# Kernel tuning notes

Hardware: AMD Instinct MI355X
Metric: run time of the kernel (lower is better)

## Reference

```python
import jax, jax.numpy as jnp
import numpy as np

L, H, P = 32768, 512, 256


def setup_inputs() -> dict:
    key = jax.random.key(0)
    ks = jax.random.split(key, 9)
    sH = 1.0 / np.sqrt(H).astype(np.float32)
    sP = 1.0 / np.sqrt(P).astype(np.float32)
    return {
        "input_sequence": jax.random.normal(ks[0], (L, H), jnp.float32),
        "Lambda_re": jax.random.normal(ks[1], (P,), jnp.float32),
        "Lambda_im": jax.random.normal(ks[2], (P,), jnp.float32) * np.float32(np.pi),
        "B_re": jax.random.normal(ks[3], (P, H), jnp.float32) * sH,
        "B_im": jax.random.normal(ks[4], (P, H), jnp.float32) * sH,
        "C_re": jax.random.normal(ks[5], (H, P), jnp.float32) * sP,
        "C_im": jax.random.normal(ks[6], (H, P), jnp.float32) * sP,
        "D": jax.random.normal(ks[7], (H,), jnp.float32),
        "log_step": jax.random.normal(ks[8], (P,), jnp.float32) - 3.0,
    }


def reference(input_sequence, Lambda_re, Lambda_im, B_re, B_im, C_re, C_im, D, log_step):
    # clip_eigs=True: enforce left-half-plane eigenvalues
    Lambda = jnp.clip(Lambda_re, None, -1e-4) + 1j * Lambda_im          # (P,)
    B_tilde = B_re + 1j * B_im                                          # (P,H)
    C_tilde = C_re + 1j * C_im                                          # (H,P)
    step = jnp.exp(log_step)                                            # step_rescale = 1.0, (P,)

    # ZOH discretization
    Lambda_bar = jnp.exp(Lambda * step)                                 # (P,) complex64
    B_bar = ((Lambda_bar - 1.0) / Lambda)[:, None] * B_tilde            # (P,H) complex64

    # Bu_elements: (L,P) complex; equivalent to vmap(lambda u: B_bar @ u)
    Bu = input_sequence.astype(B_bar.dtype) @ B_bar.T                   # (L,P)
    Lambda_elems = jnp.broadcast_to(Lambda_bar, (input_sequence.shape[0], Lambda_bar.shape[0]))

    def binop(q_i, q_j):
        A_i, b_i = q_i
        A_j, b_j = q_j
        return A_j * A_i, A_j * b_i + b_j

    _, xs = jax.lax.associative_scan(binop, (Lambda_elems, Bu))         # xs: (L,P)

    # conj_sym=True: ys = 2 * Re(C_tilde @ x) per step
    ys = 2.0 * (xs @ C_tilde.T).real                                    # (L,H)
    return ys + D * input_sequence
```

## Files before the change

kernel.cpp:

```cpp
#include <hip/hip_runtime.h>
#include <cstdint>
#include <cstddef>

typedef __bf16 bf16x8 __attribute__((ext_vector_type(8)));
typedef float f32x4 __attribute__((ext_vector_type(4)));

#define L_SEQ 32768
#define H_DIM 512
#define P_DIM 256
#define NP2   512
#define CHUNK 32
#define NCHUNK 1024
#define NSUPER 32

__device__ __forceinline__ void gload_lds16(const void* g, void* l) {
    __builtin_amdgcn_global_load_lds(
        (const __attribute__((address_space(1))) void*)g,
        (__attribute__((address_space(3))) void*)l,
        16, 0, 0);
}

__global__ void prep_kernel(const float* __restrict__ Lre, const float* __restrict__ Lim,
                            const float* __restrict__ lstep, float* __restrict__ par) {
    int p = threadIdx.x;
    if (p >= P_DIM) return;
    float lr = fminf(Lre[p], -1e-4f);
    float li = Lim[p];
    float st = expf(lstep[p]);
    float ldr = lr * st;
    float ldi = li * st;
    float er = expf(ldr);
    float ar = er * cosf(ldi);
    float ai = er * sinf(ldi);
    float den = lr * lr + li * li;
    float mr = ar - 1.0f, mi = ai;
    float cr = (mr * lr + mi * li) / den;
    float ci = (mi * lr - mr * li) / den;
    float e32  = expf((float)CHUNK * ldr);
    float ph32 = (float)CHUNK * ldi;
    float pr = e32 * cosf(ph32);
    float pi = e32 * sinf(ph32);
    par[p] = ar;        par[256 + p] = ai;
    par[512 + p] = cr;  par[768 + p] = ci;
    par[1024 + p] = pr; par[1280 + p] = pi;
    par[1536 + p] = ldr; par[1792 + p] = ldi;
}

__global__ void build_B_kernel(const float* __restrict__ Bre, const float* __restrict__ Bim,
                               const float* __restrict__ par, __bf16* __restrict__ Bt) {
    int idx = blockIdx.x * blockDim.x + threadIdx.x;
    int p = idx >> 9;
    int h = idx & 511;
    float cr = par[512 + p], ci = par[768 + p];
    float br = Bre[idx], bi = Bim[idx];
    Bt[(size_t)p * NP2 + h]         = (__bf16)(cr * br - ci * bi);
    Bt[(size_t)(256 + p) * NP2 + h] = (__bf16)(cr * bi + ci * br);
}

__global__ void build_C_kernel(const float* __restrict__ Cre, const float* __restrict__ Cim,
                               __bf16* __restrict__ Ct) {
    int idx = blockIdx.x * blockDim.x + threadIdx.x;
    int h = idx >> 8;
    int q = idx & 255;
    Ct[(size_t)h * NP2 + q]       = (__bf16)( 2.0f * Cre[idx]);
    Ct[(size_t)h * NP2 + 256 + q] = (__bf16)(-2.0f * Cim[idx]);
}

__global__ void cast_u_kernel(const float4* __restrict__ in, bf16x8* __restrict__ out, int n8) {
    int i = blockIdx.x * blockDim.x + threadIdx.x;
    if (i >= n8) return;
    float4 a = in[2 * i], b = in[2 * i + 1];
    bf16x8 v;
    v[0] = (__bf16)a.x; v[1] = (__bf16)a.y; v[2] = (__bf16)a.z; v[3] = (__bf16)a.w;
    v[4] = (__bf16)b.x; v[5] = (__bf16)b.y; v[6] = (__bf16)b.z; v[7] = (__bf16)b.w;
    out[i] = v;
}

template<bool FUSE>
__global__ __launch_bounds__(256)
void gemm_bt_kernel(const __bf16* __restrict__ A, const __bf16* __restrict__ Bt,
                    void* __restrict__ CoutV, const float* __restrict__ Dvec,
                    const float* __restrict__ U) {
    const int K = NP2, N = NP2;
    __shared__ __align__(16) __bf16 As[2][128 * 64];
    __shared__ __align__(16) __bf16 Bs[2][128 * 64];
    const int t = threadIdx.x;
    const int l = t & 63;
    const int w = t >> 6;
    const int wr = w >> 1, wc = w & 1;
    const int b    = blockIdx.x;
    const int n_sw = (b & 7) * 128 + (b >> 3);
    const int row0 = (n_sw >> 2) * 128;
    const int col0 = (n_sw & 3) * 128;
    const int lr = l & 15;
    const int lk = (l >> 4) * 8;
    f32x4 acc[4][4] = {};

    auto STAGE = [&](int buf, int k0) {
#pragma unroll
        for (int i = 0; i < 4; ++i) {
            int off = i * 256 + t;
            int r  = off >> 3;
            int ce = ((off & 7) ^ (r & 7)) * 8;
            gload_lds16(A  + (size_t)(row0 + r) * K + (k0 + ce), &As[buf][off * 8]);
            gload_lds16(Bt + (size_t)(col0 + r) * K + (k0 + ce), &Bs[buf][off * 8]);
        }
    };

    auto COMPUTE = [&](int buf) {
#pragma unroll
        for (int kk = 0; kk < 64; kk += 32) {
            bf16x8 a[4], b2[4];
            const int ls = (kk + lk) >> 3;
#pragma unroll
            for (int m = 0; m < 4; ++m) {
                int row = wr * 64 + m * 16 + lr;
                a[m] = *reinterpret_cast<const bf16x8*>(&As[buf][row * 64 + ((ls ^ (row & 7)) << 3)]);
            }
#pragma unroll
            for (int n = 0; n < 4; ++n) {
                int row = wc * 64 + n * 16 + lr;
                b2[n] = *reinterpret_cast<const bf16x8*>(&Bs[buf][row * 64 + ((ls ^ (row & 7)) << 3)]);
            }
            __builtin_amdgcn_s_setprio(1);
#pragma unroll
            for (int m = 0; m < 4; ++m)
#pragma unroll
                for (int n = 0; n < 4; ++n)
                    acc[m][n] = __builtin_amdgcn_mfma_f32_16x16x32_bf16(a[m], b2[n], acc[m][n], 0, 0, 0);
            __builtin_amdgcn_s_setprio(0);
        }
    };

    STAGE(0, 0);
    int cur = 0;
#pragma unroll
    for (int k0 = 64; k0 < K; k0 += 64) {
        STAGE(cur ^ 1, k0);
        asm volatile("s_waitcnt vmcnt(8)" ::: "memory");
        __builtin_amdgcn_s_barrier();
        __builtin_amdgcn_sched_barrier(0);
        COMPUTE(cur);
        __builtin_amdgcn_sched_barrier(0);
        __builtin_amdgcn_s_barrier();
        __builtin_amdgcn_sched_barrier(0);
        cur ^= 1;
    }
    asm volatile("s_waitcnt vmcnt(0)" ::: "memory");
    __builtin_amdgcn_s_barrier();
    __builtin_amdgcn_sched_barrier(0);
    COMPUTE(cur);

    const int lg = (l >> 4) * 4;
#pragma unroll
    for (int m = 0; m < 4; ++m) {
#pragma unroll
        for (int n = 0; n < 4; ++n) {
            int col = col0 + wc * 64 + n * 16 + lr;
#pragma unroll
            for (int j = 0; j < 4; ++j) {
                int row = row0 + wr * 64 + m * 16 + lg + j;
                size_t o = (size_t)row * N + col;
                if (FUSE) {
                    ((float*)CoutV)[o] = acc[m][n][j] + Dvec[col] * U[o];
                } else {
                    ((__bf16*)CoutV)[o] = (__bf16)acc[m][n][j];
                }
            }
        }
    }
}

__global__ void scanA_kernel(const __bf16* __restrict__ Bu, const float* __restrict__ par,
                             float* __restrict__ Fr, float* __restrict__ Fi) {
    int g = blockIdx.x;
    int p = threadIdx.x;
    float ar = par[p], ai = par[256 + p];
    const __bf16* bu = Bu + (size_t)g * CHUNK * NP2;
    float xr = 0.f, xi = 0.f;
#pragma unroll 4
    for (int i = 0; i < CHUNK; ++i) {
        float br = (float)bu[i * NP2 + p];
        float bi = (float)bu[i * NP2 + 256 + p];
        float nr = fmaf(ar, xr, fmaf(-ai, xi, br));
        float ni = fmaf(ar, xi, fmaf( ai, xr, bi));
        xr = nr; xi = ni;
    }
    Fr[g * 256 + p] = xr;
    Fi[g * 256 + p] = xi;
}

__global__ void scanB1_kernel(const float* __restrict__ Fr, const float* __restrict__ Fi,
                              const float* __restrict__ par,
                              float* __restrict__ Lr, float* __restrict__ Li,
                              float* __restrict__ Tr, float* __restrict__ Ti) {
    int s = blockIdx.x;
    int p = threadIdx.x;
    float pr = par[1024 + p], pi = par[1280 + p];
    float er = 0.f, ei = 0.f;
    int base = s * 32;
#pragma unroll
    for (int j = 0; j < 32; ++j) {
        int g = base + j;
        Lr[g * 256 + p] = er;
        Li[g * 256 + p] = ei;
        float fr = Fr[g * 256 + p], fi = Fi[g * 256 + p];
        float nr = fmaf(pr, er, fmaf(-pi, ei, fr));
        float ni = fmaf(pr, ei, fmaf( pi, er, fi));
        er = nr; ei = ni;
    }
    Tr[s * 256 + p] = er;
    Ti[s * 256 + p] = ei;
}

__global__ void scanB2_kernel(const float* __restrict__ Tr, const float* __restrict__ Ti,
                              const float* __restrict__ par,
                              float* __restrict__ Er, float* __restrict__ Ei) {
    int p = threadIdx.x;
    float ldr = par[1536 + p], ldi = par[1792 + p];
    float e  = expf(1024.0f * ldr);
    float ph = 1024.0f * ldi;
    float qr = e * cosf(ph), qi = e * sinf(ph);
    float er = 0.f, ei = 0.f;
#pragma unroll
    for (int s = 0; s < NSUPER; ++s) {
        Er[s * 256 + p] = er;
        Ei[s * 256 + p] = ei;
        float fr = Tr[s * 256 + p], fi = Ti[s * 256 + p];
        float nr = fmaf(qr, er, fmaf(-qi, ei, fr));
        float ni = fmaf(qr, ei, fmaf( qi, er, fi));
        er = nr; ei = ni;
    }
}

__global__ void scanC_kernel(const __bf16* __restrict__ Bu, const float* __restrict__ par,
                             const float* __restrict__ Lr, const float* __restrict__ Li,
                             const float* __restrict__ Er, const float* __restrict__ Ei,
                             __bf16* __restrict__ xs) {
    int g = blockIdx.x;
    int p = threadIdx.x;
    int s = g >> 5, k = g & 31;
    float ar = par[p], ai = par[256 + p];
    float ldr = par[1536 + p], ldi = par[1792 + p];
    float kk = (float)(32 * k);
    float e  = expf(kk * ldr);
    float ph = kk * ldi;
    float qr = e * cosf(ph), qi = e * sinf(ph);
    float er = Er[s * 256 + p], ei = Ei[s * 256 + p];
    float lr0 = Lr[g * 256 + p], li0 = Li[g * 256 + p];
    float xr = fmaf(qr, er, fmaf(-qi, ei, lr0));
    float xi = fmaf(qr, ei, fmaf( qi, er, li0));
    const __bf16* bu = Bu + (size_t)g * CHUNK * NP2;
    __bf16* xo = xs + (size_t)g * CHUNK * NP2;
#pragma unroll 4
    for (int i = 0; i < CHUNK; ++i) {
        float br = (float)bu[i * NP2 + p];
        float bi = (float)bu[i * NP2 + 256 + p];
        float nr = fmaf(ar, xr, fmaf(-ai, xi, br));
        float ni = fmaf(ar, xi, fmaf( ai, xr, bi));
        xr = nr; xi = ni;
        xo[i * NP2 + p]       = (__bf16)xr;
        xo[i * NP2 + 256 + p] = (__bf16)xi;
    }
}

extern "C" void kernel_launch(void* const* d_in, const int* in_sizes, int n_in,
                              void* d_out, int out_size, void* d_ws, size_t ws_size,
                              hipStream_t stream) {
    const float* u   = (const float*)d_in[0];
    const float* Lre = (const float*)d_in[1];
    const float* Lim = (const float*)d_in[2];
    const float* Bre = (const float*)d_in[3];
    const float* Bim = (const float*)d_in[4];
    const float* Cre = (const float*)d_in[5];
    const float* Cim = (const float*)d_in[6];
    const float* Dv  = (const float*)d_in[7];
    const float* lst = (const float*)d_in[8];

    char* w = (char*)d_ws;
    size_t off = 0;
    float* par = (float*)(w + off);      off += 16 * 1024;
    __bf16* Btm = (__bf16*)(w + off);    off += (size_t)NP2 * NP2 * 2;
    __bf16* Ctm = (__bf16*)(w + off);    off += (size_t)NP2 * NP2 * 2;
    float* Fr  = (float*)(w + off);      off += (size_t)NCHUNK * 256 * 4;
    float* Fi  = (float*)(w + off);      off += (size_t)NCHUNK * 256 * 4;
    float* Lr  = (float*)(w + off);      off += (size_t)NCHUNK * 256 * 4;
    float* Li  = (float*)(w + off);      off += (size_t)NCHUNK * 256 * 4;
    float* Tr  = (float*)(w + off);      off += (size_t)NSUPER * 256 * 4;
    float* Ti  = (float*)(w + off);      off += (size_t)NSUPER * 256 * 4;
    float* Er  = (float*)(w + off);      off += (size_t)NSUPER * 256 * 4;
    float* Ei  = (float*)(w + off);      off += (size_t)NSUPER * 256 * 4;
    __bf16* Ubf = (__bf16*)(w + off);    off += (size_t)L_SEQ * H_DIM * 2;
    if (ws_size < off) return;

    __bf16* Bu = (__bf16*)d_out;

    prep_kernel   <<<1,    256, 0, stream>>>(Lre, Lim, lst, par);
    build_B_kernel<<<512,  256, 0, stream>>>(Bre, Bim, par, Btm);
    build_C_kernel<<<512,  256, 0, stream>>>(Cre, Cim, Ctm);
    cast_u_kernel <<<8192, 256, 0, stream>>>((const float4*)u, (bf16x8*)Ubf, L_SEQ * H_DIM / 8);
    gemm_bt_kernel<false><<<1024, 256, 0, stream>>>(Ubf, Btm, (void*)Bu, nullptr, nullptr);
    scanA_kernel  <<<NCHUNK, 256, 0, stream>>>(Bu, par, Fr, Fi);
    scanB1_kernel <<<NSUPER, 256, 0, stream>>>(Fr, Fi, par, Lr, Li, Tr, Ti);
    scanB2_kernel <<<1,      256, 0, stream>>>(Tr, Ti, par, Er, Ei);
    scanC_kernel  <<<NCHUNK, 256, 0, stream>>>(Bu, par, Lr, Li, Er, Ei, Ubf);
    gemm_bt_kernel<true><<<1024, 256, 0, stream>>>(Ubf, Ctm, d_out, Dv, u);
}
```

Baseline: 108.7 us.

## Single-buffer B tile in GEMM, split staging, read bf16 input in epilogue

The GEMM keeps A double-buffered but drops B to a single LDS buffer. B is now loaded at the start of each k-step alongside the prefetch of the next A tile, and the peeled final iteration is folded into the loop. This halves B's LDS footprint and may improve occupancy, but B loads are no longer overlapped with the previous compute. The scan output now goes to a separate Xs workspace so the bf16 copy of u survives, and the fused epilogue reads that bf16 u instead of fp32 u, halving epilogue read traffic at a small cost in precision on the D*u term.

Result: faster. 104.1 us (-4.2%).

```diff
diff --git a/kernel.cpp b/kernel.cpp
--- a/kernel.cpp
+++ b/kernel.cpp
@@ -80,10 +80,10 @@
 __global__ __launch_bounds__(256)
 void gemm_bt_kernel(const __bf16* __restrict__ A, const __bf16* __restrict__ Bt,
                     void* __restrict__ CoutV, const float* __restrict__ Dvec,
-                    const float* __restrict__ U) {
+                    const __bf16* __restrict__ Ubf) {
     const int K = NP2, N = NP2;
     __shared__ __align__(16) __bf16 As[2][128 * 64];
-    __shared__ __align__(16) __bf16 Bs[2][128 * 64];
+    __shared__ __align__(16) __bf16 Bs[128 * 64];
     const int t = threadIdx.x;
     const int l = t & 63;
     const int w = t >> 6;
@@ -96,14 +96,22 @@
     const int lk = (l >> 4) * 8;
     f32x4 acc[4][4] = {};
 
-    auto STAGE = [&](int buf, int k0) {
+    auto STAGE_A = [&](int buf, int k0) {
 #pragma unroll
         for (int i = 0; i < 4; ++i) {
             int off = i * 256 + t;
             int r  = off >> 3;
             int ce = ((off & 7) ^ (r & 7)) * 8;
-            gload_lds16(A  + (size_t)(row0 + r) * K + (k0 + ce), &As[buf][off * 8]);
-            gload_lds16(Bt + (size_t)(col0 + r) * K + (k0 + ce), &Bs[buf][off * 8]);
+            gload_lds16(A + (size_t)(row0 + r) * K + (k0 + ce), &As[buf][off * 8]);
+        }
+    };
+    auto STAGE_B = [&](int k0) {
+#pragma unroll
+        for (int i = 0; i < 4; ++i) {
+            int off = i * 256 + t;
+            int r  = off >> 3;
+            int ce = ((off & 7) ^ (r & 7)) * 8;
+            gload_lds16(Bt + (size_t)(col0 + r) * K + (k0 + ce), &Bs[off * 8]);
         }
     };
 
@@ -120,7 +128,7 @@
 #pragma unroll
             for (int n = 0; n < 4; ++n) {
                 int row = wc * 64 + n * 16 + lr;
-                b2[n] = *reinterpret_cast<const bf16x8*>(&Bs[buf][row * 64 + ((ls ^ (row & 7)) << 3)]);
+                b2[n] = *reinterpret_cast<const bf16x8*>(&Bs[row * 64 + ((ls ^ (row & 7)) << 3)]);
             }
             __builtin_amdgcn_s_setprio(1);
 #pragma unroll
@@ -132,24 +140,24 @@
         }
     };
 
-    STAGE(0, 0);
+    STAGE_A(0, 0);
     int cur = 0;
 #pragma unroll
-    for (int k0 = 64; k0 < K; k0 += 64) {
-        STAGE(cur ^ 1, k0);
-        asm volatile("s_waitcnt vmcnt(8)" ::: "memory");
+    for (int k0 = 0; k0 < K; k0 += 64) {
+        STAGE_B(k0);
+        if (k0 + 64 < K) {
+            STAGE_A(cur ^ 1, k0 + 64);
+            asm volatile("s_waitcnt vmcnt(4)" ::: "memory");
+        } else {
+            asm volatile("s_waitcnt vmcnt(0)" ::: "memory");
+        }
         __builtin_amdgcn_s_barrier();
         __builtin_amdgcn_sched_barrier(0);
         COMPUTE(cur);
         __builtin_amdgcn_sched_barrier(0);
         __builtin_amdgcn_s_barrier();
-        __builtin_amdgcn_sched_barrier(0);
         cur ^= 1;
     }
-    asm volatile("s_waitcnt vmcnt(0)" ::: "memory");
-    __builtin_amdgcn_s_barrier();
-    __builtin_amdgcn_sched_barrier(0);
-    COMPUTE(cur);
 
     const int lg = (l >> 4) * 4;
 #pragma unroll
@@ -162,7 +170,7 @@
                 int row = row0 + wr * 64 + m * 16 + lg + j;
                 size_t o = (size_t)row * N + col;
                 if (FUSE) {
-                    ((float*)CoutV)[o] = acc[m][n][j] + Dvec[col] * U[o];
+                    ((float*)CoutV)[o] = acc[m][n][j] + Dvec[col] * (float)Ubf[o];
                 } else {
                     ((__bf16*)CoutV)[o] = (__bf16)acc[m][n][j];
                 }
@@ -291,6 +299,7 @@
     float* Er  = (float*)(w + off);      off += (size_t)NSUPER * 256 * 4;
     float* Ei  = (float*)(w + off);      off += (size_t)NSUPER * 256 * 4;
     __bf16* Ubf = (__bf16*)(w + off);    off += (size_t)L_SEQ * H_DIM * 2;
+    __bf16* Xs  = (__bf16*)(w + off);    off += (size_t)L_SEQ * NP2 * 2;
     if (ws_size < off) return;
 
     __bf16* Bu = (__bf16*)d_out;
@@ -303,6 +312,6 @@
     scanA_kernel  <<<NCHUNK, 256, 0, stream>>>(Bu, par, Fr, Fi);
     scanB1_kernel <<<NSUPER, 256, 0, stream>>>(Fr, Fi, par, Lr, Li, Tr, Ti);
     scanB2_kernel <<<1,      256, 0, stream>>>(Tr, Ti, par, Er, Ei);
-    scanC_kernel  <<<NCHUNK, 256, 0, stream>>>(Bu, par, Lr, Li, Er, Ei, Ubf);
-    gemm_bt_kernel<true><<<1024, 256, 0, stream>>>(Ubf, Ctm, d_out, Dv, u);
-}
+    scanC_kernel  <<<NCHUNK, 256, 0, stream>>>(Bu, par, Lr, Li, Er, Ei, Xs);
+    gemm_bt_kernel<true><<<1024, 256, 0, stream>>>(Xs, Ctm, d_out, Dv, Ubf);
+}
```
